# Kernel tuning notes

Measured on AMD Instinct MI355X. Metric: run time of the kernel, lower is better.

The kernel has to match this reference:

```python
import jax, jax.numpy as jnp
import numpy as np

IMAGE_W = 1024
IMAGE_H = 1024
MIN_SCORE_THRESHOLD = 0.05
NMS_THRESHOLD = 0.5
MAX_DETECTION_NUM = 100


def setup_inputs() -> dict:
    key = jax.random.key(0)
    k1, k2, k3, k4 = jax.random.split(key, 4)
    B, N, C = 2, 8192, 80
    cls_heads = jax.random.uniform(k1, (B, N, C), jnp.float32)          # post-sigmoid class probs
    reg_heads = jax.random.normal(k2, (B, N, 4), jnp.float32)           # tx,ty,tw,th
    ctr = jax.random.uniform(k3, (B, N, 2), jnp.float32, 0.0, 1024.0)   # anchor centers
    wh = jax.random.uniform(k4, (B, N, 2), jnp.float32, 16.0, 256.0)    # anchor sizes
    anchors = jnp.concatenate([ctr - 0.5 * wh, ctr + 0.5 * wh], axis=-1)  # x1,y1,x2,y2
    return {"cls_heads": cls_heads, "reg_heads": reg_heads, "anchors": anchors}


def _snap_boxes(reg, anchors):
    # reg, anchors: [N, 4]
    awh = anchors[:, 2:] - anchors[:, :2]
    actr = anchors[:, :2] + 0.5 * awh
    factor = jnp.array([0.1, 0.1, 0.2, 0.2], dtype=reg.dtype)
    reg = reg * factor
    pwh = jnp.exp(reg[:, 2:]) * awh
    pctr = reg[:, :2] * awh + actr
    boxes = jnp.concatenate([pctr - 0.5 * pwh, pctr + 0.5 * pwh], axis=1)
    boxes = jax.lax.stop_gradient(boxes).astype(jnp.int32)  # torch .int() truncation
    boxes = boxes.at[:, 0].set(jnp.maximum(boxes[:, 0], 0))
    boxes = boxes.at[:, 1].set(jnp.maximum(boxes[:, 1], 0))
    boxes = boxes.at[:, 2].set(jnp.minimum(boxes[:, 2], IMAGE_W - 1))
    boxes = boxes.at[:, 3].set(jnp.minimum(boxes[:, 3], IMAGE_H - 1))
    return boxes


def _decode_one(cls_head, reg_head, anchor):
    # cls_head: [N, C], reg_head: [N, 4], anchor: [N, 4]
    scores = jnp.max(cls_head, axis=-1)
    classes = jnp.argmax(cls_head, axis=-1).astype(jnp.int32)
    boxes = _snap_boxes(reg_head, anchor)  # int32 [N,4]
    valid = scores > MIN_SCORE_THRESHOLD

    order = jnp.argsort(-scores)  # descending score order
    s = scores[order]
    c = classes[order]
    b = boxes[order]
    v = valid[order]

    bf = b.astype(jnp.float32)
    x1, y1, x2, y2 = bf[:, 0], bf[:, 1], bf[:, 2], bf[:, 3]
    area = jnp.maximum(x2 - x1, 0.0) * jnp.maximum(y2 - y1, 0.0)
    ix1 = jnp.maximum(x1[:, None], x1[None, :])
    iy1 = jnp.maximum(y1[:, None], y1[None, :])
    ix2 = jnp.minimum(x2[:, None], x2[None, :])
    iy2 = jnp.minimum(y2[:, None], y2[None, :])
    inter = jnp.maximum(ix2 - ix1, 0.0) * jnp.maximum(iy2 - iy1, 0.0)
    union = area[:, None] + area[None, :] - inter
    iou = jnp.where(union > 0.0, inter / union, 0.0)  # [N,N]

    N = s.shape[0]
    idx = jnp.arange(N)
    # class-wise suppression: box j (lower score) suppressed by kept box i if IoU>thr
    sup = (iou > NMS_THRESHOLD) & (c[:, None] == c[None, :]) & (idx[None, :] > idx[:, None])

    def body(i, keep):
        return jnp.where(keep[i], keep & ~sup[i], keep)

    keep = jax.lax.fori_loop(0, N, body, v)

    final_scores = jnp.where(keep, s, -1.0)
    top_s, top_i = jax.lax.top_k(final_scores, MAX_DETECTION_NUM)
    ok = top_s > -0.5
    out_scores = jnp.where(ok, top_s, -1.0)
    out_classes = jnp.where(ok, c[top_i], -1)
    out_boxes = jnp.where(ok[:, None], b[top_i], -1)
    return out_scores, out_classes, out_boxes


def reference(cls_heads, reg_heads, anchors):
    # cls_heads: [B,N,C], reg_heads: [B,N,4], anchors: [B,N,4]
    return jax.vmap(_decode_one)(cls_heads, reg_heads, anchors)
```

## Files before the change

kernel.cpp:

```cpp
#include <hip/hip_runtime.h>
#include <stdint.h>

#define NANCH   8192
#define NCLS    80
#define IMW     1024
#define IMH     1024
#define MAXDET  100
#define SCORE_TH 0.05f
#define TAU      0.999691f
#define CAP      512
#define KSENT    0x7FFFFFF0
#define ROWS_PB  64

__device__ __forceinline__ float key_score(uint64_t key) {
    uint32_t m = (uint32_t)(key >> 32);
    uint32_t bits = (m & 0x80000000u) ? (m & 0x7FFFFFFFu) : ~m;
    return __uint_as_float(bits);
}

__device__ __forceinline__ void decode_one(const float4 r, const float4 a,
                                           uint32_t mono32, int bj, int n,
                                           uint64_t& key, uint64_t& meta) {
    float awx = __fsub_rn(a.z, a.x);
    float awy = __fsub_rn(a.w, a.y);
    float acx = __fadd_rn(a.x, __fmul_rn(0.5f, awx));
    float acy = __fadd_rn(a.y, __fmul_rn(0.5f, awy));
    float rx = __fmul_rn(r.x, 0.1f);
    float ry = __fmul_rn(r.y, 0.1f);
    float rw = __fmul_rn(r.z, 0.2f);
    float rh = __fmul_rn(r.w, 0.2f);
    float pwx = __fmul_rn(expf(rw), awx);
    float pwy = __fmul_rn(expf(rh), awy);
    float pcx = __fadd_rn(__fmul_rn(rx, awx), acx);
    float pcy = __fadd_rn(__fmul_rn(ry, awy), acy);

    int x1 = (int)__fsub_rn(pcx, __fmul_rn(0.5f, pwx));
    int y1 = (int)__fsub_rn(pcy, __fmul_rn(0.5f, pwy));
    int x2 = (int)__fadd_rn(pcx, __fmul_rn(0.5f, pwx));
    int y2 = (int)__fadd_rn(pcy, __fmul_rn(0.5f, pwy));
    x1 = max(x1, 0);
    y1 = max(y1, 0);
    x2 = min(x2, IMW - 1);
    y2 = min(y2, IMH - 1);

    key = ((uint64_t)mono32 << 32)
        | ((uint64_t)((~(uint32_t)n) & 0xFFFFu) << 16)
        | (uint64_t)(uint32_t)bj;
    meta = (uint64_t)(uint16_t)x1
         | ((uint64_t)(uint16_t)y1 << 16)
         | ((uint64_t)(uint16_t)x2 << 32)
         | ((uint64_t)(uint16_t)y2 << 48);
}

__global__ __launch_bounds__(256)
void decode_kernel(const float* __restrict__ cls_heads,
                   const float* __restrict__ reg_heads,
                   const float* __restrict__ anchors,
                   int* __restrict__ cnt,
                   ulonglong2* __restrict__ surv) {
    const int tid  = threadIdx.x;
    const int lane = tid & 63;
    const int part = tid & 3;
    const int b    = blockIdx.y;
    const int n    = blockIdx.x * ROWS_PB + (tid >> 2);
    const int row  = b * NANCH + n;

    float best = -1e30f; int bestj = 0;
    {
        const float* rp = cls_heads + (size_t)row * NCLS;
#pragma unroll
        for (int k = 0; k < 5; ++k) {
            int j0 = part * 4 + k * 16;
            float4 v = *reinterpret_cast<const float4*>(rp + j0);
            if (v.x > best) { best = v.x; bestj = j0 + 0; }
            if (v.y > best) { best = v.y; bestj = j0 + 1; }
            if (v.z > best) { best = v.z; bestj = j0 + 2; }
            if (v.w > best) { best = v.w; bestj = j0 + 3; }
        }
    }
    uint32_t ub = __float_as_uint(best);
    uint32_t mono = (ub & 0x80000000u) ? ~ub : (ub | 0x80000000u);
    uint64_t kk = ((uint64_t)mono << 8) | (uint64_t)(255 - bestj);
    {
        uint64_t o = __shfl_xor(kk, 1); if (o > kk) kk = o;
        o = __shfl_xor(kk, 2); if (o > kk) kk = o;
    }

    uint64_t key = 0, meta = 0;
    bool svv = false;
    if (part == 0) {
        uint32_t mono32 = (uint32_t)(kk >> 8);
        uint32_t mono_tau = __float_as_uint(TAU) | 0x80000000u;
        if (mono32 > mono_tau) {
            int bj = 255 - (int)(kk & 0xFF);
            float4 r = reinterpret_cast<const float4*>(reg_heads)[row];
            float4 a = reinterpret_cast<const float4*>(anchors)[row];
            decode_one(r, a, mono32, bj, n, key, meta);
            svv = true;
        }
    }

    uint64_t mask = __ballot(svv);
    int rank = __popcll(mask & ((1ULL << lane) - 1ULL));
    int base = 0;
    if (lane == 0 && mask) base = atomicAdd(cnt + b, __popcll(mask));
    base = __shfl(base, 0);
    if (svv) {
        int p = base + rank;
        if (p < CAP) surv[(size_t)b * CAP + p] = make_ulonglong2(key, meta);
    }
}

struct Kept {
    float x1[2], y1[2], x2[2], y2[2], ar[2];
    int   cl[2];
};

__device__ __forceinline__ void nms_try_keep(uint64_t key, uint64_t meta, float s,
                                             int lane, int& nk, Kept& K,
                                             float* __restrict__ out, int b) {
    int cls = (int)(key & 0xFFFFu);
    float cx1 = (float)(short)(meta & 0xFFFFu);
    float cy1 = (float)(short)((meta >> 16) & 0xFFFFu);
    float cx2 = (float)(short)((meta >> 32) & 0xFFFFu);
    float cy2 = (float)(short)((meta >> 48) & 0xFFFFu);
    float ca = fmaxf(cx2 - cx1, 0.f) * fmaxf(cy2 - cy1, 0.f);

    bool supp = false;
#pragma unroll
    for (int r = 0; r < 2; ++r) {
        int slot = lane + 64 * r;
        if (slot < nk && K.cl[r] == cls) {
            float ix1 = fmaxf(K.x1[r], cx1), iy1 = fmaxf(K.y1[r], cy1);
            float ix2 = fminf(K.x2[r], cx2), iy2 = fminf(K.y2[r], cy2);
            float inter = fmaxf(ix2 - ix1, 0.f) * fmaxf(iy2 - iy1, 0.f);
            if (3.f * inter > K.ar[r] + ca) supp = true;
        }
    }
    if (__ballot(supp) != 0ULL) return;

    int rr = nk >> 6, l = nk & 63;
    if (lane == l) {
        if (rr == 0) { K.x1[0]=cx1; K.y1[0]=cy1; K.x2[0]=cx2; K.y2[0]=cy2; K.ar[0]=ca; K.cl[0]=cls; }
        else         { K.x1[1]=cx1; K.y1[1]=cy1; K.x2[1]=cx2; K.y2[1]=cy2; K.ar[1]=ca; K.cl[1]=cls; }
    }
    if (lane == 0) {
        out[b * MAXDET + nk] = s;
        out[2 * MAXDET + b * MAXDET + nk] = (float)cls;
        float* ob = out + 4 * MAXDET + (size_t)(b * MAXDET + nk) * 4;
        ob[0] = cx1; ob[1] = cy1; ob[2] = cx2; ob[3] = cy2;
    }
    ++nk;
}

__global__ __launch_bounds__(256)
void sort_nms_kernel(const int* __restrict__ cnt,
                     const float* __restrict__ cls_heads,
                     const float* __restrict__ reg_heads,
                     const float* __restrict__ anchors,
                     uint64_t* __restrict__ wk,
                     uint64_t* __restrict__ wm,
                     const ulonglong2* __restrict__ surv,
                     float* __restrict__ out) {
    __shared__ __align__(16) ulonglong2 sq[CAP];
    __shared__ __align__(16) uint64_t skey[CAP + 16];
    __shared__ float4 kept_box[128];
    __shared__ float  kept_area[128];
    __shared__ int    kept_cls[128];
    __shared__ uint64_t smask[4];
    __shared__ uint64_t sby[4 * 64];
    __shared__ int snk, sdone, sneedfb;
    __shared__ uint64_t fbmap[NANCH / 64];

    const int b = blockIdx.x;
    const int tid = threadIdx.x;
    const int lane = tid & 63;
    const int w = tid >> 6;

    ulonglong2 v0 = surv[(size_t)b * CAP + tid];
    ulonglong2 v1 = surv[(size_t)b * CAP + 256 + tid];
    int c = cnt[b];

    bool overflow = (c > CAP) || (c < 0);
    if (overflow) c = 0;
    const int cpad   = (c + 63) & ~63;
    const int cpad16 = (c + 15) & ~15;

    skey[tid]       = (tid < c)       ? v0.x : 0ULL;
    skey[256 + tid] = (256 + tid < c) ? v1.x : 0ULL;
    if (tid < 128) kept_cls[tid] = KSENT;
    if (tid == 0) { snk = 0; sdone = 0; sneedfb = overflow ? 1 : 0; }
    __syncthreads();

    {
        bool h0 = tid < c, h1 = 256 + tid < c;
        if (h0 | h1) {
            uint64_t k0 = v0.x, k1 = v1.x;
            int r0 = 0, r1 = 0;
            for (int j0 = 0; j0 < cpad16; j0 += 16) {
#pragma unroll
                for (int u = 0; u < 8; ++u) {
                    ulonglong2 pr = *reinterpret_cast<const ulonglong2*>(&skey[j0 + 2 * u]);
                    r0 += (int)(pr.x > k0) + (int)(pr.y > k0);
                    r1 += (int)(pr.x > k1) + (int)(pr.y > k1);
                }
            }
            if (h0) sq[r0] = v0;
            if (h1) sq[r1] = v1;
        }
    }
    for (int i = c + tid; i < cpad; i += 256) sq[i] = make_ulonglong2(0ULL, 0ULL);

    for (int p0 = 0; p0 < cpad; p0 += 64) {
        __syncthreads();
        if (sdone) break;
        const int nk = snk;

        ulonglong2 kv = sq[p0 + lane];
        uint64_t key = kv.x, meta = kv.y;
        float s = key_score(key);
        bool sval = (s > SCORE_TH);
        int cls_c = sval ? (int)(key & 0xFFFFu) : -1;
        float cx1 = (float)(short)(meta & 0xFFFFu);
        float cy1 = (float)(short)((meta >> 16) & 0xFFFFu);
        float cx2 = (float)(short)((meta >> 32) & 0xFFFFu);
        float cy2 = (float)(short)((meta >> 48) & 0xFFFFu);
        float ca = fmaxf(cx2 - cx1, 0.f) * fmaxf(cy2 - cy1, 0.f);

        bool supk = false;
        int kp = (((nk + 3) >> 2) + 7) & ~7;
        for (int k0 = 0; k0 < kp; k0 += 8) {
#pragma unroll
            for (int u = 0; u < 8; ++u) {
                int j = w + 4 * (k0 + u);
                float4 kb = kept_box[j];
                float ka = kept_area[j];
                int kc = kept_cls[j];
                float ix1 = fmaxf(kb.x, cx1), iy1 = fmaxf(kb.y, cy1);
                float ix2 = fminf(kb.z, cx2), iy2 = fminf(kb.w, cy2);
                float inter = fmaxf(ix2 - ix1, 0.f) * fmaxf(iy2 - iy1, 0.f);
                supk |= (kc == cls_c) & (3.f * inter > ka + ca);
            }
        }

        uint64_t sbyw = 0;
#pragma unroll
        for (int u = 0; u < 16; ++u) {
            int t = (w << 4) + u;
            ulonglong2 tv = sq[p0 + t];
            uint64_t tkey = tv.x, tmeta = tv.y;
            float ts = key_score(tkey);
            int tcls = (int)(tkey & 0xFFFFu);
            float tx1 = (float)(short)(tmeta & 0xFFFFu);
            float ty1 = (float)(short)((tmeta >> 16) & 0xFFFFu);
            float tx2 = (float)(short)((tmeta >> 32) & 0xFFFFu);
            float ty2 = (float)(short)((tmeta >> 48) & 0xFFFFu);
            float ta = fmaxf(tx2 - tx1, 0.f) * fmaxf(ty2 - ty1, 0.f);
            float ix1 = fmaxf(tx1, cx1), iy1 = fmaxf(ty1, cy1);
            float ix2 = fminf(tx2, cx2), iy2 = fminf(ty2, cy2);
            float inter = fmaxf(ix2 - ix1, 0.f) * fmaxf(iy2 - iy1, 0.f);
            bool sup = (t < lane) && (ts > SCORE_TH) && (tcls == cls_c)
                       && (3.f * inter > ta + ca);
            sbyw |= ((uint64_t)sup) << t;
        }

        uint64_t mk = __ballot(supk);
        if (lane == 0) smask[w] = mk;
        sby[(w << 6) + lane] = sbyw;
        __syncthreads();

        if (w == 0) {
            uint64_t supkAll = smask[0] | smask[1] | smask[2] | smask[3];
            uint64_t supBy = sby[lane] | sby[64 + lane] | sby[128 + lane] | sby[192 + lane];
            bool alive0 = sval && !((supkAll >> lane) & 1ULL);

            uint64_t aliveCand = __ballot(alive0);
            uint64_t aliveMask;
            if (__ballot(supBy != 0ULL) == 0ULL) {
                aliveMask = aliveCand;
            } else {
                uint64_t killed = 0;
                for (int t = 0; t < 64; ++t) {
                    uint64_t kill_t = __ballot((supBy >> t) & 1ULL);
                    bool talive = ((aliveCand >> t) & 1ULL) && !((killed >> t) & 1ULL);
                    if (talive) killed |= kill_t;
                }
                aliveMask = aliveCand & ~killed;
            }

            int myrank = __popcll(aliveMask & ((1ULL << lane) - 1ULL));
            bool keepme = ((aliveMask >> lane) & 1ULL) && (nk + myrank < MAXDET);
            if (keepme) {
                int slot = nk + myrank;
                kept_box[slot]  = make_float4(cx1, cy1, cx2, cy2);
                kept_area[slot] = ca;
                kept_cls[slot]  = cls_c;
                out[b * MAXDET + slot] = s;
                out[2 * MAXDET + b * MAXDET + slot] = (float)cls_c;
                float* ob = out + 4 * MAXDET + (size_t)(b * MAXDET + slot) * 4;
                ob[0] = cx1; ob[1] = cy1; ob[2] = cx2; ob[3] = cy2;
            }
            int navail = __popcll(aliveMask);
            int room = MAXDET - nk;
            int nk2 = nk + ((navail < room) ? navail : room);
            uint64_t invalid = __ballot(!sval);
            if (lane == 0) {
                snk = nk2;
                if (nk2 >= MAXDET) sdone = 1;
                else if (invalid) { sneedfb = 1; sdone = 1; }
            }
        }
    }
    __syncthreads();

    int nk = snk;
    bool need_fb = sneedfb || (!sdone && nk < MAXDET);

    if (need_fb) {
        uint64_t* wkb = wk + (size_t)b * NANCH;
        uint64_t* wmb = wm + (size_t)b * NANCH;
        for (int n2 = tid; n2 < NANCH; n2 += 256) {
            int row2 = b * NANCH + n2;
            const float* rp = cls_heads + (size_t)row2 * NCLS;
            float best = -1e30f; int bj = 0;
            for (int j = 0; j < NCLS; ++j) {
                float v = rp[j];
                if (v > best) { best = v; bj = j; }
            }
            uint32_t ub = __float_as_uint(best);
            uint32_t mono32 = (ub & 0x80000000u) ? ~ub : (ub | 0x80000000u);
            float4 r = reinterpret_cast<const float4*>(reg_heads)[row2];
            float4 a = reinterpret_cast<const float4*>(anchors)[row2];
            uint64_t key2, meta2;
            decode_one(r, a, mono32, bj, n2, key2, meta2);
            wkb[n2] = key2;
            wmb[n2] = meta2;
        }
        __syncthreads();
    }

    if (tid >= 64) return;

    if (need_fb) {
        const uint64_t* wkb = wk + (size_t)b * NANCH;
        const uint64_t* wmb = wm + (size_t)b * NANCH;
        for (int i = lane; i < NANCH / 64; i += 64) fbmap[i] = 0ULL;
        __builtin_amdgcn_wave_barrier();

        nk = 0;
        Kept K;
        K.cl[0] = K.cl[1] = -1;
        K.x1[0]=K.y1[0]=K.x2[0]=K.y2[0]=K.ar[0]=0.f;
        K.x1[1]=K.y1[1]=K.x2[1]=K.y2[1]=K.ar[1]=0.f;

        for (int iter = 0; iter < NANCH; ++iter) {
            uint64_t mybest = 0; int myq = -1;
            for (int q = lane; q < NANCH; q += 64) {
                bool cons = (fbmap[q >> 6] >> (q & 63)) & 1ULL;
                uint64_t kk2 = wkb[q];
                if (!cons && kk2 > mybest) { mybest = kk2; myq = q; }
            }
            uint64_t best2 = mybest;
#pragma unroll
            for (int j = 32; j; j >>= 1) {
                uint64_t o = __shfl_xor(best2, j);
                if (o > best2) best2 = o;
            }
            if (best2 == 0ULL) break;
            float s = key_score(best2);
            if (!(s > SCORE_TH)) break;
            uint64_t msk = __ballot(mybest == best2);
            int wl = __ffsll((unsigned long long)msk) - 1;
            int q = __shfl(myq, wl);
            if (lane == wl) fbmap[q >> 6] |= (1ULL << (q & 63));
            uint64_t cm = wmb[q];
            nms_try_keep(best2, cm, s, lane, nk, K, out, b);
            if (nk == MAXDET) break;
            __builtin_amdgcn_wave_barrier();
        }
    }

    for (int t = nk + lane; t < MAXDET; t += 64) {
        out[b * MAXDET + t] = -1.f;
        out[2 * MAXDET + b * MAXDET + t] = -1.f;
        float* ob = out + 4 * MAXDET + (size_t)(b * MAXDET + t) * 4;
        ob[0] = -1.f; ob[1] = -1.f; ob[2] = -1.f; ob[3] = -1.f;
    }
}

extern "C" void kernel_launch(void* const* d_in, const int* in_sizes, int n_in,
                              void* d_out, int out_size, void* d_ws, size_t ws_size,
                              hipStream_t stream) {
    (void)in_sizes; (void)n_in; (void)out_size; (void)ws_size;
    const float* cls_heads = (const float*)d_in[0];
    const float* reg_heads = (const float*)d_in[1];
    const float* anchors   = (const float*)d_in[2];
    float* out = (float*)d_out;

    char* w = (char*)d_ws;
    int*        cnt  = (int*)w;
    uint64_t*   wk   = (uint64_t*)(w + 1024);
    uint64_t*   wm   = (uint64_t*)(w + 1024 + 131072);
    ulonglong2* surv = (ulonglong2*)(w + 1024 + 262144);

    hipMemsetAsync(cnt, 0, 2 * sizeof(int), stream);
    decode_kernel<<<dim3(NANCH / ROWS_PB, 2), 256, 0, stream>>>(cls_heads, reg_heads, anchors,
                                                                cnt, surv);
    sort_nms_kernel<<<dim3(2), 256, 0, stream>>>(cnt, cls_heads, reg_heads, anchors,
                                                 wk, wm, surv, out);
}
```

Measured before the change: 25.34 us.

## Run greedy NMS chunks in a single wavefront and halve candidate capacity

```diff
diff --git a/kernel.cpp b/kernel.cpp
--- a/kernel.cpp
+++ b/kernel.cpp
@@ -8,7 +8,7 @@
 #define MAXDET  100
 #define SCORE_TH 0.05f
 #define TAU      0.999691f
-#define CAP      512
+#define CAP      256
 #define KSENT    0x7FFFFFF0
 #define ROWS_PB  64
 
@@ -167,18 +167,16 @@
     __shared__ float4 kept_box[128];
     __shared__ float  kept_area[128];
     __shared__ int    kept_cls[128];
-    __shared__ uint64_t smask[4];
-    __shared__ uint64_t sby[4 * 64];
-    __shared__ int snk, sdone, sneedfb;
+    __shared__ float4 sbox[64];
+    __shared__ float  sarea[64];
+    __shared__ int    scls[64];
     __shared__ uint64_t fbmap[NANCH / 64];
 
     const int b = blockIdx.x;
     const int tid = threadIdx.x;
     const int lane = tid & 63;
-    const int w = tid >> 6;
 
     ulonglong2 v0 = surv[(size_t)b * CAP + tid];
-    ulonglong2 v1 = surv[(size_t)b * CAP + 256 + tid];
     int c = cnt[b];
 
     bool overflow = (c > CAP) || (c < 0);
@@ -186,36 +184,34 @@
     const int cpad   = (c + 63) & ~63;
     const int cpad16 = (c + 15) & ~15;
 
-    skey[tid]       = (tid < c)       ? v0.x : 0ULL;
-    skey[256 + tid] = (256 + tid < c) ? v1.x : 0ULL;
+    skey[tid] = (tid < c) ? v0.x : 0ULL;
     if (tid < 128) kept_cls[tid] = KSENT;
-    if (tid == 0) { snk = 0; sdone = 0; sneedfb = overflow ? 1 : 0; }
     __syncthreads();
 
-    {
-        bool h0 = tid < c, h1 = 256 + tid < c;
-        if (h0 | h1) {
-            uint64_t k0 = v0.x, k1 = v1.x;
-            int r0 = 0, r1 = 0;
-            for (int j0 = 0; j0 < cpad16; j0 += 16) {
-#pragma unroll
-                for (int u = 0; u < 8; ++u) {
-                    ulonglong2 pr = *reinterpret_cast<const ulonglong2*>(&skey[j0 + 2 * u]);
-                    r0 += (int)(pr.x > k0) + (int)(pr.y > k0);
-                    r1 += (int)(pr.x > k1) + (int)(pr.y > k1);
-                }
-            }
-            if (h0) sq[r0] = v0;
-            if (h1) sq[r1] = v1;
-        }
+    if (tid < c) {
+        uint64_t k0 = v0.x;
+        int r = 0;
+        for (int j0 = 0; j0 < cpad16; j0 += 16) {
+            int acc = 0;
+#pragma unroll
+            for (int u = 0; u < 8; ++u) {
+                ulonglong2 pr = *reinterpret_cast<const ulonglong2*>(&skey[j0 + 2 * u]);
+                acc += (int)(pr.x > k0) + (int)(pr.y > k0);
+            }
+            r += acc;
+        }
+        sq[r] = v0;
     }
     for (int i = c + tid; i < cpad; i += 256) sq[i] = make_ulonglong2(0ULL, 0ULL);
-
-    for (int p0 = 0; p0 < cpad; p0 += 64) {
-        __syncthreads();
-        if (sdone) break;
-        const int nk = snk;
-
+    __syncthreads();
+
+    if (tid >= 64) return;
+
+    int nk = 0;
+    bool done = false;
+    bool need_fb = overflow;
+
+    for (int p0 = 0; p0 < cpad && !done; p0 += 64) {
         ulonglong2 kv = sq[p0 + lane];
         uint64_t key = kv.x, meta = kv.y;
         float s = key_score(key);
@@ -227,99 +223,85 @@
         float cy2 = (float)(short)((meta >> 48) & 0xFFFFu);
         float ca = fmaxf(cx2 - cx1, 0.f) * fmaxf(cy2 - cy1, 0.f);
 
+        sbox[lane]  = make_float4(cx1, cy1, cx2, cy2);
+        sarea[lane] = ca;
+        scls[lane]  = sval ? (int)(key & 0xFFFFu) : 0x7FFF;
+        __builtin_amdgcn_wave_barrier();
+
         bool supk = false;
-        int kp = (((nk + 3) >> 2) + 7) & ~7;
-        for (int k0 = 0; k0 < kp; k0 += 8) {
+        int nkp = (nk + 7) & ~7;
+        for (int j0 = 0; j0 < nkp; j0 += 8) {
 #pragma unroll
             for (int u = 0; u < 8; ++u) {
-                int j = w + 4 * (k0 + u);
-                float4 kb = kept_box[j];
-                float ka = kept_area[j];
-                int kc = kept_cls[j];
+                float4 kb = kept_box[j0 + u];
+                float ka = kept_area[j0 + u];
+                int kc = kept_cls[j0 + u];
                 float ix1 = fmaxf(kb.x, cx1), iy1 = fmaxf(kb.y, cy1);
                 float ix2 = fminf(kb.z, cx2), iy2 = fminf(kb.w, cy2);
                 float inter = fmaxf(ix2 - ix1, 0.f) * fmaxf(iy2 - iy1, 0.f);
                 supk |= (kc == cls_c) & (3.f * inter > ka + ca);
             }
         }
-
-        uint64_t sbyw = 0;
-#pragma unroll
-        for (int u = 0; u < 16; ++u) {
-            int t = (w << 4) + u;
-            ulonglong2 tv = sq[p0 + t];
-            uint64_t tkey = tv.x, tmeta = tv.y;
-            float ts = key_score(tkey);
-            int tcls = (int)(tkey & 0xFFFFu);
-            float tx1 = (float)(short)(tmeta & 0xFFFFu);
-            float ty1 = (float)(short)((tmeta >> 16) & 0xFFFFu);
-            float tx2 = (float)(short)((tmeta >> 32) & 0xFFFFu);
-            float ty2 = (float)(short)((tmeta >> 48) & 0xFFFFu);
-            float ta = fmaxf(tx2 - tx1, 0.f) * fmaxf(ty2 - ty1, 0.f);
-            float ix1 = fmaxf(tx1, cx1), iy1 = fmaxf(ty1, cy1);
-            float ix2 = fminf(tx2, cx2), iy2 = fminf(ty2, cy2);
-            float inter = fmaxf(ix2 - ix1, 0.f) * fmaxf(iy2 - iy1, 0.f);
-            bool sup = (t < lane) && (ts > SCORE_TH) && (tcls == cls_c)
-                       && (3.f * inter > ta + ca);
-            sbyw |= ((uint64_t)sup) << t;
-        }
-
-        uint64_t mk = __ballot(supk);
-        if (lane == 0) smask[w] = mk;
-        sby[(w << 6) + lane] = sbyw;
-        __syncthreads();
-
-        if (w == 0) {
-            uint64_t supkAll = smask[0] | smask[1] | smask[2] | smask[3];
-            uint64_t supBy = sby[lane] | sby[64 + lane] | sby[128 + lane] | sby[192 + lane];
-            bool alive0 = sval && !((supkAll >> lane) & 1ULL);
-
-            uint64_t aliveCand = __ballot(alive0);
-            uint64_t aliveMask;
-            if (__ballot(supBy != 0ULL) == 0ULL) {
-                aliveMask = aliveCand;
-            } else {
-                uint64_t killed = 0;
-                for (int t = 0; t < 64; ++t) {
-                    uint64_t kill_t = __ballot((supBy >> t) & 1ULL);
-                    bool talive = ((aliveCand >> t) & 1ULL) && !((killed >> t) & 1ULL);
-                    if (talive) killed |= kill_t;
-                }
-                aliveMask = aliveCand & ~killed;
-            }
-
-            int myrank = __popcll(aliveMask & ((1ULL << lane) - 1ULL));
-            bool keepme = ((aliveMask >> lane) & 1ULL) && (nk + myrank < MAXDET);
-            if (keepme) {
-                int slot = nk + myrank;
-                kept_box[slot]  = make_float4(cx1, cy1, cx2, cy2);
-                kept_area[slot] = ca;
-                kept_cls[slot]  = cls_c;
-                out[b * MAXDET + slot] = s;
-                out[2 * MAXDET + b * MAXDET + slot] = (float)cls_c;
-                float* ob = out + 4 * MAXDET + (size_t)(b * MAXDET + slot) * 4;
-                ob[0] = cx1; ob[1] = cy1; ob[2] = cx2; ob[3] = cy2;
-            }
-            int navail = __popcll(aliveMask);
-            int room = MAXDET - nk;
-            int nk2 = nk + ((navail < room) ? navail : room);
-            uint64_t invalid = __ballot(!sval);
-            if (lane == 0) {
-                snk = nk2;
-                if (nk2 >= MAXDET) sdone = 1;
-                else if (invalid) { sneedfb = 1; sdone = 1; }
-            }
-        }
-    }
-    __syncthreads();
-
-    int nk = snk;
-    bool need_fb = sneedfb || (!sdone && nk < MAXDET);
+        bool alive0 = sval && !supk;
+
+        uint64_t supBy = 0;
+        for (int t0 = 0; t0 < 64; t0 += 8) {
+#pragma unroll
+            for (int u = 0; u < 8; ++u) {
+                int t = t0 + u;
+                float4 tb = sbox[t];
+                float ta = sarea[t];
+                int tcls = scls[t];
+                float ix1 = fmaxf(tb.x, cx1), iy1 = fmaxf(tb.y, cy1);
+                float ix2 = fminf(tb.z, cx2), iy2 = fminf(tb.w, cy2);
+                float inter = fmaxf(ix2 - ix1, 0.f) * fmaxf(iy2 - iy1, 0.f);
+                bool sup = (t < lane) && (tcls == cls_c) && (3.f * inter > ta + ca);
+                supBy |= ((uint64_t)sup) << t;
+            }
+        }
+
+        uint64_t aliveCand = __ballot(alive0);
+        uint64_t aliveMask;
+        if (__ballot(supBy != 0ULL) == 0ULL) {
+            aliveMask = aliveCand;
+        } else {
+            uint64_t killed = 0;
+            for (int t = 0; t < 64; ++t) {
+                uint64_t kill_t = __ballot((supBy >> t) & 1ULL);
+                bool talive = ((aliveCand >> t) & 1ULL) && !((killed >> t) & 1ULL);
+                if (talive) killed |= kill_t;
+            }
+            aliveMask = aliveCand & ~killed;
+        }
+
+        int myrank = __popcll(aliveMask & ((1ULL << lane) - 1ULL));
+        bool keepme = ((aliveMask >> lane) & 1ULL) && (nk + myrank < MAXDET);
+        if (keepme) {
+            int slot = nk + myrank;
+            kept_box[slot]  = make_float4(cx1, cy1, cx2, cy2);
+            kept_area[slot] = ca;
+            kept_cls[slot]  = cls_c;
+            out[b * MAXDET + slot] = s;
+            out[2 * MAXDET + b * MAXDET + slot] = (float)cls_c;
+            float* ob = out + 4 * MAXDET + (size_t)(b * MAXDET + slot) * 4;
+            ob[0] = cx1; ob[1] = cy1; ob[2] = cx2; ob[3] = cy2;
+        }
+        __builtin_amdgcn_wave_barrier();
+
+        int navail = __popcll(aliveMask);
+        int room = MAXDET - nk;
+        nk += (navail < room) ? navail : room;
+
+        uint64_t invalid = __ballot(!sval);
+        if (nk >= MAXDET) done = true;
+        else if (invalid) { need_fb = true; done = true; }
+    }
+    if (!done && nk < MAXDET) need_fb = true;
 
     if (need_fb) {
         uint64_t* wkb = wk + (size_t)b * NANCH;
         uint64_t* wmb = wm + (size_t)b * NANCH;
-        for (int n2 = tid; n2 < NANCH; n2 += 256) {
+        for (int n2 = lane; n2 < NANCH; n2 += 64) {
             int row2 = b * NANCH + n2;
             const float* rp = cls_heads + (size_t)row2 * NCLS;
             float best = -1e30f; int bj = 0;
@@ -336,14 +318,6 @@
             wkb[n2] = key2;
             wmb[n2] = meta2;
         }
-        __syncthreads();
-    }
-
-    if (tid >= 64) return;
-
-    if (need_fb) {
-        const uint64_t* wkb = wk + (size_t)b * NANCH;
-        const uint64_t* wmb = wm + (size_t)b * NANCH;
         for (int i = lane; i < NANCH / 64; i += 64) fbmap[i] = 0ULL;
         __builtin_amdgcn_wave_barrier();
 
```

Result: slower. 31.28 us (+23.4%).
